# Optimization experiments

Measured on AMD Instinct MI355X. Metric: run time of the kernel, lower is better.

The kernel has to match this reference:

```python
import jax, jax.numpy as jnp
import numpy as np

B, M, D, HOPS = 32, 8192, 128, 3
NEG_BIG = -1e10  # matches (1 - memory_mask) * -1e10 in the original


def setup_inputs() -> dict:
    key = jax.random.key(0)
    k = jax.random.split(key, 6)
    return {
        "query_vector": jax.random.normal(k[0], (B, D), dtype=jnp.float32),
        # m_story[h] is the hop-h memory (already summed over token axis and gated upstream)
        "m_story": jax.random.normal(k[1], (HOPS + 1, B, M, D), dtype=jnp.float32),
        "global_pointer": jax.random.uniform(k[2], (B, M), dtype=jnp.float32),
        "local_attention": jax.random.uniform(k[3], (B, M), dtype=jnp.float32),
        "reason_mask": jax.random.randint(k[4], (B, M), 0, 2, dtype=jnp.int32),
        "memory_mask": jax.random.randint(k[5], (B, M), 0, 2, dtype=jnp.int32),
    }


def reference(query_vector, m_story, global_pointer, local_attention, reason_mask, memory_mask):
    # gating applied to both m_A and m_C every hop (ablationG off, attention=True)
    gate = (global_pointer * local_attention)[:, :, None]        # [B, M, 1]
    allowed = reason_mask.astype(bool)                           # rea=True: positions in `reason`
    mm = memory_mask.astype(jnp.float32)                         # [B, M]
    u = query_vector                                             # [B, D]
    n_hops = m_story.shape[0] - 1
    for hop in range(n_hops):
        m_A = m_story[hop] * gate                                # [B, M, D]
        prob_logits = jnp.einsum('bmd,bd->bm', m_A, u)           # [B, M]
        prob_logits = jnp.where(allowed, prob_logits, -jnp.inf)  # reason mask (vectorized double-loop)
        prob_logits = prob_logits + (1.0 - mm) * NEG_BIG
        prob_soft = jax.nn.softmax(prob_logits, axis=1)          # softmax over memory dim
        m_C = m_story[hop + 1] * gate                            # [B, M, D]
        o_k = jnp.einsum('bm,bmd->bd', prob_soft, m_C)           # [B, D]
        u = u + o_k
    return prob_soft, prob_logits, u
```

## Files before the change

### kernel.cpp

```cpp
#include <hip/hip_runtime.h>
#include <math.h>

constexpr int Bc = 32;
constexpr int Mc = 8192;
constexpr int Dc = 128;
constexpr int NHOPS = 3;
constexpr float NEGBIG = -1e10f;
constexpr float SENT = -3.0e38f;

constexpr int ROWS = 256;
constexpr int BLK_PER_B = Mc / ROWS;

__global__ __launch_bounds__(256) void k_init_u(const float* __restrict__ q,
                                                float* __restrict__ u) {
    int i = blockIdx.x * 256 + threadIdx.x;
    if (i < Bc * Dc) u[i] = q[i];
}

__global__ __launch_bounds__(256) void k_logits(
    const float* __restrict__ ms_hop,
    const float* __restrict__ u,
    const float* __restrict__ gp,
    const float* __restrict__ la,
    const int*   __restrict__ rmask,
    const int*   __restrict__ mmask,
    float* __restrict__ logits,
    float* __restrict__ ws_stats)
{
    const int b   = blockIdx.y;
    const int m0  = blockIdx.x * ROWS;
    const int tid = threadIdx.x;
    const int lane = tid & 31, grp = tid >> 5;
    const int wv = tid >> 6, wl = tid & 63;

    __shared__ alignas(16) float u_s[Dc];
    __shared__ float logit_s[ROWS];
    __shared__ float gate_s[ROWS];
    __shared__ float bias_s[ROWS];
    __shared__ short list_s[ROWS];
    __shared__ int   wcnt[4];
    __shared__ float red_s[256];

    if (tid < Dc) u_s[tid] = u[b * Dc + tid];
    const int idx = b * Mc + m0 + tid;
    const bool keep = rmask[idx] != 0;
    gate_s[tid]  = gp[idx] * la[idx];
    bias_s[tid]  = (1.0f - (float)mmask[idx]) * NEGBIG;
    logit_s[tid] = SENT;
    {
        unsigned long long bm_ = __ballot(keep);
        int pfx = __popcll(bm_ & ((1ull << wl) - 1ull));
        if (wl == 0) wcnt[wv] = __popcll(bm_);
        __syncthreads();
        int base = 0;
        for (int w2 = 0; w2 < wv; ++w2) base += wcnt[w2];
        if (keep) list_s[base + pfx] = (short)tid;
    }
    __syncthreads();
    const int cnt = wcnt[0] + wcnt[1] + wcnt[2] + wcnt[3];
    const float4 u4 = ((const float4*)u_s)[lane];

    int i = grp;
    for (; i + 8 < cnt; i += 16) {
        const int r0 = list_s[i], r1 = list_s[i + 8];
        const float4 v0 = ((const float4*)(ms_hop + (size_t)(m0 + r0) * Dc))[lane];
        const float4 v1 = ((const float4*)(ms_hop + (size_t)(m0 + r1) * Dc))[lane];
        float d0 = v0.x * u4.x + v0.y * u4.y + v0.z * u4.z + v0.w * u4.w;
        float d1 = v1.x * u4.x + v1.y * u4.y + v1.z * u4.z + v1.w * u4.w;
        #pragma unroll
        for (int off = 16; off > 0; off >>= 1) {
            d0 += __shfl_xor(d0, off, 32);
            d1 += __shfl_xor(d1, off, 32);
        }
        if (lane == 0) {
            logit_s[r0] = d0 * gate_s[r0] + bias_s[r0];
            logit_s[r1] = d1 * gate_s[r1] + bias_s[r1];
        }
    }
    for (; i < cnt; i += 8) {
        const int r0 = list_s[i];
        const float4 v0 = ((const float4*)(ms_hop + (size_t)(m0 + r0) * Dc))[lane];
        float d0 = v0.x * u4.x + v0.y * u4.y + v0.z * u4.z + v0.w * u4.w;
        #pragma unroll
        for (int off = 16; off > 0; off >>= 1) d0 += __shfl_xor(d0, off, 32);
        if (lane == 0) logit_s[r0] = d0 * gate_s[r0] + bias_s[r0];
    }
    __syncthreads();

    logits[idx] = logit_s[tid];
    red_s[tid] = logit_s[tid];
    __syncthreads();
    for (int s = 128; s > 0; s >>= 1) {
        if (tid < s) red_s[tid] = fmaxf(red_s[tid], red_s[tid + s]);
        __syncthreads();
    }
    const float M = red_s[0];
    __syncthreads();
    red_s[tid] = expf(logit_s[tid] - M);
    __syncthreads();
    for (int s = 128; s > 0; s >>= 1) {
        if (tid < s) red_s[tid] += red_s[tid + s];
        __syncthreads();
    }
    if (tid == 0) {
        const int blk = b * BLK_PER_B + blockIdx.x;
        ws_stats[blk * 2 + 0] = M;
        ws_stats[blk * 2 + 1] = red_s[0];
    }
}

__global__ __launch_bounds__(256) void k_accum(
    const float* __restrict__ ms_next,
    const float* __restrict__ logits,
    const float* __restrict__ gp,
    const float* __restrict__ la,
    const float* __restrict__ ws_stats,
    float* __restrict__ prob,
    float* __restrict__ u,
    int last)
{
    const int b   = blockIdx.y;
    const int m0  = blockIdx.x * ROWS;
    const int tid = threadIdx.x;
    const int lane = tid & 31, grp = tid >> 5;
    const int wv = tid >> 6, wl = tid & 63;

    __shared__ float w_s[ROWS];
    __shared__ short list_s[ROWS];
    __shared__ int   wcnt[4];
    __shared__ float sm_s[BLK_PER_B], ss_s[BLK_PER_B];
    __shared__ float bstat[2];
    __shared__ alignas(16) float acc_s[8 * Dc];

    if (tid < BLK_PER_B) {
        sm_s[tid] = ws_stats[(b * BLK_PER_B + tid) * 2 + 0];
        ss_s[tid] = ws_stats[(b * BLK_PER_B + tid) * 2 + 1];
    }
    __syncthreads();
    if (tid == 0) {
        float M = -INFINITY, S = 0.0f;
        for (int c = 0; c < BLK_PER_B; ++c) M = fmaxf(M, sm_s[c]);
        for (int c = 0; c < BLK_PER_B; ++c) S += ss_s[c] * expf(sm_s[c] - M);
        bstat[0] = M;
        bstat[1] = 1.0f / S;
    }
    __syncthreads();
    const float bm = bstat[0], inv = bstat[1];

    const int idx = b * Mc + m0 + tid;
    const float p = expf(logits[idx] - bm) * inv;
    if (last) prob[idx] = p;
    const float w = p * gp[idx] * la[idx];
    w_s[tid] = w;
    {
        const bool nz = (w != 0.0f);
        unsigned long long bm_ = __ballot(nz);
        int pfx = __popcll(bm_ & ((1ull << wl) - 1ull));
        if (wl == 0) wcnt[wv] = __popcll(bm_);
        __syncthreads();
        int base = 0;
        for (int w2 = 0; w2 < wv; ++w2) base += wcnt[w2];
        if (nz) list_s[base + pfx] = (short)tid;
    }
    __syncthreads();
    const int cnt = wcnt[0] + wcnt[1] + wcnt[2] + wcnt[3];

    float4 acc = make_float4(0.f, 0.f, 0.f, 0.f);
    int i = grp;
    for (; i + 8 < cnt; i += 16) {
        const int r0 = list_s[i], r1 = list_s[i + 8];
        const float w0 = w_s[r0], w1 = w_s[r1];
        const float4 v0 = ((const float4*)(ms_next + (size_t)(m0 + r0) * Dc))[lane];
        const float4 v1 = ((const float4*)(ms_next + (size_t)(m0 + r1) * Dc))[lane];
        acc.x += w0 * v0.x; acc.y += w0 * v0.y;
        acc.z += w0 * v0.z; acc.w += w0 * v0.w;
        acc.x += w1 * v1.x; acc.y += w1 * v1.y;
        acc.z += w1 * v1.z; acc.w += w1 * v1.w;
    }
    for (; i < cnt; i += 8) {
        const int r0 = list_s[i];
        const float w0 = w_s[r0];
        const float4 v0 = ((const float4*)(ms_next + (size_t)(m0 + r0) * Dc))[lane];
        acc.x += w0 * v0.x; acc.y += w0 * v0.y;
        acc.z += w0 * v0.z; acc.w += w0 * v0.w;
    }
    ((float4*)(acc_s + grp * Dc))[lane] = acc;
    __syncthreads();

    if (tid < Dc) {
        float s = 0.0f;
        #pragma unroll
        for (int g = 0; g < 8; ++g) s += acc_s[g * Dc + tid];
        atomicAdd(&u[b * Dc + tid], s);
    }
}

extern "C" void kernel_launch(void* const* d_in, const int* in_sizes, int n_in,
                              void* d_out, int out_size, void* d_ws,
                              size_t ws_size, hipStream_t stream) {
    const float* q  = (const float*)d_in[0];
    const float* ms = (const float*)d_in[1];
    const float* gp = (const float*)d_in[2];
    const float* la = (const float*)d_in[3];
    const int*   rm = (const int*)d_in[4];
    const int*   mm = (const int*)d_in[5];

    float* out_prob   = (float*)d_out;
    float* out_logits = out_prob + (size_t)Bc * Mc;
    float* out_u      = out_logits + (size_t)Bc * Mc;

    float* ws_stats = (float*)d_ws;

    k_init_u<<<dim3((Bc * Dc + 255) / 256), dim3(256), 0, stream>>>(q, out_u);

    for (int hop = 0; hop < NHOPS; ++hop) {
        const float* ms_h = ms + (size_t)hop       * Bc * Mc * Dc;
        const float* ms_n = ms + (size_t)(hop + 1) * Bc * Mc * Dc;
        const int last = (hop == NHOPS - 1) ? 1 : 0;

        k_logits<<<dim3(BLK_PER_B, Bc), dim3(256), 0, stream>>>(
            ms_h, out_u, gp, la, rm, mm, out_logits, ws_stats);
        k_accum<<<dim3(BLK_PER_B, Bc), dim3(256), 0, stream>>>(
            ms_n, out_logits, gp, la, ws_stats, out_prob, out_u, last);
    }
}
```

Measured before the change: 622.7 us.

## Fuse all hops into one cooperative persistent kernel with grid syncs

Replaces the init kernel and the six per-hop logits/accumulate launches with a single cooperative kernel. It keeps gate, bias, mask lists and logits in shared memory across hops and uses grid.sync between phases. It also swaps the tree reductions for wave shuffles and unrolls the row loops to four rows. This removes launch gaps and global round-trips of logits, gp and la, but needs all 1024 blocks co-resident and pays for several grid-wide barriers.

```diff
diff --git a/kernel.cpp b/kernel.cpp
--- a/kernel.cpp
+++ b/kernel.cpp
@@ -1,5 +1,8 @@
 #include <hip/hip_runtime.h>
+#include <hip/hip_cooperative_groups.h>
 #include <math.h>
+
+namespace cg = cooperative_groups;
 
 constexpr int Bc = 32;
 constexpr int Mc = 8192;
@@ -11,22 +14,19 @@
 constexpr int ROWS = 256;
 constexpr int BLK_PER_B = Mc / ROWS;
 
-__global__ __launch_bounds__(256) void k_init_u(const float* __restrict__ q,
-                                                float* __restrict__ u) {
-    int i = blockIdx.x * 256 + threadIdx.x;
-    if (i < Bc * Dc) u[i] = q[i];
-}
-
-__global__ __launch_bounds__(256) void k_logits(
-    const float* __restrict__ ms_hop,
-    const float* __restrict__ u,
+__global__ __launch_bounds__(256, 4) void k_fused(
+    const float* __restrict__ ms,
+    const float* __restrict__ q,
     const float* __restrict__ gp,
     const float* __restrict__ la,
     const int*   __restrict__ rmask,
     const int*   __restrict__ mmask,
-    float* __restrict__ logits,
+    float* __restrict__ out_prob,
+    float* __restrict__ out_logits,
+    float* __restrict__ u,
     float* __restrict__ ws_stats)
 {
+    cg::grid_group grid = cg::this_grid();
     const int b   = blockIdx.y;
     const int m0  = blockIdx.x * ROWS;
     const int tid = threadIdx.x;
@@ -34,19 +34,21 @@
     const int wv = tid >> 6, wl = tid & 63;
 
     __shared__ alignas(16) float u_s[Dc];
-    __shared__ float logit_s[ROWS];
     __shared__ float gate_s[ROWS];
     __shared__ float bias_s[ROWS];
+    __shared__ float logit_s[ROWS];
+    __shared__ float w_s[ROWS];
     __shared__ short list_s[ROWS];
-    __shared__ int   wcnt[4];
-    __shared__ float red_s[256];
-
-    if (tid < Dc) u_s[tid] = u[b * Dc + tid];
+    __shared__ short alist_s[ROWS];
+    __shared__ int   wcnt[4], awcnt[4];
+    __shared__ float red_s[8];
+    __shared__ float bstat[2];
+    __shared__ alignas(16) float acc_s[8 * Dc];
+
     const int idx = b * Mc + m0 + tid;
     const bool keep = rmask[idx] != 0;
-    gate_s[tid]  = gp[idx] * la[idx];
-    bias_s[tid]  = (1.0f - (float)mmask[idx]) * NEGBIG;
-    logit_s[tid] = SENT;
+    gate_s[tid] = gp[idx] * la[idx];
+    bias_s[tid] = (1.0f - (float)mmask[idx]) * NEGBIG;
     {
         unsigned long long bm_ = __ballot(keep);
         int pfx = __popcll(bm_ & ((1ull << wl) - 1ull));
@@ -56,142 +58,150 @@
         for (int w2 = 0; w2 < wv; ++w2) base += wcnt[w2];
         if (keep) list_s[base + pfx] = (short)tid;
     }
-    __syncthreads();
+    if (blockIdx.x == 0 && tid < Dc)
+        __hip_atomic_store(&u[b * Dc + tid], q[b * Dc + tid],
+                           __ATOMIC_RELAXED, __HIP_MEMORY_SCOPE_AGENT);
+    grid.sync();
     const int cnt = wcnt[0] + wcnt[1] + wcnt[2] + wcnt[3];
-    const float4 u4 = ((const float4*)u_s)[lane];
-
-    int i = grp;
-    for (; i + 8 < cnt; i += 16) {
-        const int r0 = list_s[i], r1 = list_s[i + 8];
-        const float4 v0 = ((const float4*)(ms_hop + (size_t)(m0 + r0) * Dc))[lane];
-        const float4 v1 = ((const float4*)(ms_hop + (size_t)(m0 + r1) * Dc))[lane];
-        float d0 = v0.x * u4.x + v0.y * u4.y + v0.z * u4.z + v0.w * u4.w;
-        float d1 = v1.x * u4.x + v1.y * u4.y + v1.z * u4.z + v1.w * u4.w;
+
+    for (int hop = 0; hop < NHOPS; ++hop) {
+        const float* ms_h = ms + (size_t)hop * Bc * Mc * Dc + (size_t)m0 * Dc;
+
+        if (tid < Dc)
+            u_s[tid] = __hip_atomic_load(&u[b * Dc + tid],
+                                         __ATOMIC_RELAXED, __HIP_MEMORY_SCOPE_AGENT);
+        logit_s[tid] = SENT;
+        __syncthreads();
+        const float4 u4 = ((const float4*)u_s)[lane];
+
+        int i = grp;
+        for (; i + 24 < cnt; i += 32) {
+            const int r0 = list_s[i],      r1 = list_s[i + 8];
+            const int r2 = list_s[i + 16], r3 = list_s[i + 24];
+            const float4 v0 = ((const float4*)(ms_h + (size_t)r0 * Dc))[lane];
+            const float4 v1 = ((const float4*)(ms_h + (size_t)r1 * Dc))[lane];
+            const float4 v2 = ((const float4*)(ms_h + (size_t)r2 * Dc))[lane];
+            const float4 v3 = ((const float4*)(ms_h + (size_t)r3 * Dc))[lane];
+            float d0 = v0.x * u4.x + v0.y * u4.y + v0.z * u4.z + v0.w * u4.w;
+            float d1 = v1.x * u4.x + v1.y * u4.y + v1.z * u4.z + v1.w * u4.w;
+            float d2 = v2.x * u4.x + v2.y * u4.y + v2.z * u4.z + v2.w * u4.w;
+            float d3 = v3.x * u4.x + v3.y * u4.y + v3.z * u4.z + v3.w * u4.w;
+            #pragma unroll
+            for (int off = 16; off > 0; off >>= 1) {
+                d0 += __shfl_xor(d0, off, 32);
+                d1 += __shfl_xor(d1, off, 32);
+                d2 += __shfl_xor(d2, off, 32);
+                d3 += __shfl_xor(d3, off, 32);
+            }
+            if (lane == 0) {
+                logit_s[r0] = d0 * gate_s[r0] + bias_s[r0];
+                logit_s[r1] = d1 * gate_s[r1] + bias_s[r1];
+                logit_s[r2] = d2 * gate_s[r2] + bias_s[r2];
+                logit_s[r3] = d3 * gate_s[r3] + bias_s[r3];
+            }
+        }
+        for (; i < cnt; i += 8) {
+            const int r0 = list_s[i];
+            const float4 v0 = ((const float4*)(ms_h + (size_t)r0 * Dc))[lane];
+            float d0 = v0.x * u4.x + v0.y * u4.y + v0.z * u4.z + v0.w * u4.w;
+            #pragma unroll
+            for (int off = 16; off > 0; off >>= 1) d0 += __shfl_xor(d0, off, 32);
+            if (lane == 0) logit_s[r0] = d0 * gate_s[r0] + bias_s[r0];
+        }
+        __syncthreads();
+
+        const float v = logit_s[tid];
+        float mx = v;
         #pragma unroll
-        for (int off = 16; off > 0; off >>= 1) {
-            d0 += __shfl_xor(d0, off, 32);
-            d1 += __shfl_xor(d1, off, 32);
-        }
-        if (lane == 0) {
-            logit_s[r0] = d0 * gate_s[r0] + bias_s[r0];
-            logit_s[r1] = d1 * gate_s[r1] + bias_s[r1];
-        }
-    }
-    for (; i < cnt; i += 8) {
-        const int r0 = list_s[i];
-        const float4 v0 = ((const float4*)(ms_hop + (size_t)(m0 + r0) * Dc))[lane];
-        float d0 = v0.x * u4.x + v0.y * u4.y + v0.z * u4.z + v0.w * u4.w;
+        for (int off = 32; off > 0; off >>= 1) mx = fmaxf(mx, __shfl_xor(mx, off));
+        if (wl == 0) red_s[wv] = mx;
+        __syncthreads();
+        const float M = fmaxf(fmaxf(red_s[0], red_s[1]), fmaxf(red_s[2], red_s[3]));
+        float e = expf(v - M);
         #pragma unroll
-        for (int off = 16; off > 0; off >>= 1) d0 += __shfl_xor(d0, off, 32);
-        if (lane == 0) logit_s[r0] = d0 * gate_s[r0] + bias_s[r0];
-    }
-    __syncthreads();
-
-    logits[idx] = logit_s[tid];
-    red_s[tid] = logit_s[tid];
-    __syncthreads();
-    for (int s = 128; s > 0; s >>= 1) {
-        if (tid < s) red_s[tid] = fmaxf(red_s[tid], red_s[tid + s]);
-        __syncthreads();
-    }
-    const float M = red_s[0];
-    __syncthreads();
-    red_s[tid] = expf(logit_s[tid] - M);
-    __syncthreads();
-    for (int s = 128; s > 0; s >>= 1) {
-        if (tid < s) red_s[tid] += red_s[tid + s];
-        __syncthreads();
-    }
-    if (tid == 0) {
-        const int blk = b * BLK_PER_B + blockIdx.x;
-        ws_stats[blk * 2 + 0] = M;
-        ws_stats[blk * 2 + 1] = red_s[0];
-    }
-}
-
-__global__ __launch_bounds__(256) void k_accum(
-    const float* __restrict__ ms_next,
-    const float* __restrict__ logits,
-    const float* __restrict__ gp,
-    const float* __restrict__ la,
-    const float* __restrict__ ws_stats,
-    float* __restrict__ prob,
-    float* __restrict__ u,
-    int last)
-{
-    const int b   = blockIdx.y;
-    const int m0  = blockIdx.x * ROWS;
-    const int tid = threadIdx.x;
-    const int lane = tid & 31, grp = tid >> 5;
-    const int wv = tid >> 6, wl = tid & 63;
-
-    __shared__ float w_s[ROWS];
-    __shared__ short list_s[ROWS];
-    __shared__ int   wcnt[4];
-    __shared__ float sm_s[BLK_PER_B], ss_s[BLK_PER_B];
-    __shared__ float bstat[2];
-    __shared__ alignas(16) float acc_s[8 * Dc];
-
-    if (tid < BLK_PER_B) {
-        sm_s[tid] = ws_stats[(b * BLK_PER_B + tid) * 2 + 0];
-        ss_s[tid] = ws_stats[(b * BLK_PER_B + tid) * 2 + 1];
-    }
-    __syncthreads();
-    if (tid == 0) {
-        float M = -INFINITY, S = 0.0f;
-        for (int c = 0; c < BLK_PER_B; ++c) M = fmaxf(M, sm_s[c]);
-        for (int c = 0; c < BLK_PER_B; ++c) S += ss_s[c] * expf(sm_s[c] - M);
-        bstat[0] = M;
-        bstat[1] = 1.0f / S;
-    }
-    __syncthreads();
-    const float bm = bstat[0], inv = bstat[1];
-
-    const int idx = b * Mc + m0 + tid;
-    const float p = expf(logits[idx] - bm) * inv;
-    if (last) prob[idx] = p;
-    const float w = p * gp[idx] * la[idx];
-    w_s[tid] = w;
-    {
-        const bool nz = (w != 0.0f);
-        unsigned long long bm_ = __ballot(nz);
-        int pfx = __popcll(bm_ & ((1ull << wl) - 1ull));
-        if (wl == 0) wcnt[wv] = __popcll(bm_);
-        __syncthreads();
-        int base = 0;
-        for (int w2 = 0; w2 < wv; ++w2) base += wcnt[w2];
-        if (nz) list_s[base + pfx] = (short)tid;
-    }
-    __syncthreads();
-    const int cnt = wcnt[0] + wcnt[1] + wcnt[2] + wcnt[3];
-
-    float4 acc = make_float4(0.f, 0.f, 0.f, 0.f);
-    int i = grp;
-    for (; i + 8 < cnt; i += 16) {
-        const int r0 = list_s[i], r1 = list_s[i + 8];
-        const float w0 = w_s[r0], w1 = w_s[r1];
-        const float4 v0 = ((const float4*)(ms_next + (size_t)(m0 + r0) * Dc))[lane];
-        const float4 v1 = ((const float4*)(ms_next + (size_t)(m0 + r1) * Dc))[lane];
-        acc.x += w0 * v0.x; acc.y += w0 * v0.y;
-        acc.z += w0 * v0.z; acc.w += w0 * v0.w;
-        acc.x += w1 * v1.x; acc.y += w1 * v1.y;
-        acc.z += w1 * v1.z; acc.w += w1 * v1.w;
-    }
-    for (; i < cnt; i += 8) {
-        const int r0 = list_s[i];
-        const float w0 = w_s[r0];
-        const float4 v0 = ((const float4*)(ms_next + (size_t)(m0 + r0) * Dc))[lane];
-        acc.x += w0 * v0.x; acc.y += w0 * v0.y;
-        acc.z += w0 * v0.z; acc.w += w0 * v0.w;
-    }
-    ((float4*)(acc_s + grp * Dc))[lane] = acc;
-    __syncthreads();
-
-    if (tid < Dc) {
-        float s = 0.0f;
-        #pragma unroll
-        for (int g = 0; g < 8; ++g) s += acc_s[g * Dc + tid];
-        atomicAdd(&u[b * Dc + tid], s);
+        for (int off = 32; off > 0; off >>= 1) e += __shfl_xor(e, off);
+        if (wl == 0) red_s[4 + wv] = e;
+        if (hop == NHOPS - 1) out_logits[idx] = v;
+        __syncthreads();
+        if (tid == 0) {
+            const int blk = b * BLK_PER_B + blockIdx.x;
+            __hip_atomic_store(&ws_stats[blk * 2 + 0], M,
+                               __ATOMIC_RELAXED, __HIP_MEMORY_SCOPE_AGENT);
+            __hip_atomic_store(&ws_stats[blk * 2 + 1],
+                               red_s[4] + red_s[5] + red_s[6] + red_s[7],
+                               __ATOMIC_RELAXED, __HIP_MEMORY_SCOPE_AGENT);
+        }
+        grid.sync();
+
+        if (wv == 0) {
+            float sm = (wl < BLK_PER_B)
+                ? __hip_atomic_load(&ws_stats[(b * BLK_PER_B + wl) * 2 + 0],
+                                    __ATOMIC_RELAXED, __HIP_MEMORY_SCOPE_AGENT)
+                : -INFINITY;
+            float ss = (wl < BLK_PER_B)
+                ? __hip_atomic_load(&ws_stats[(b * BLK_PER_B + wl) * 2 + 1],
+                                    __ATOMIC_RELAXED, __HIP_MEMORY_SCOPE_AGENT)
+                : 0.0f;
+            float Mg = sm;
+            #pragma unroll
+            for (int off = 32; off > 0; off >>= 1) Mg = fmaxf(Mg, __shfl_xor(Mg, off));
+            float t = ss * expf(sm - Mg);
+            #pragma unroll
+            for (int off = 32; off > 0; off >>= 1) t += __shfl_xor(t, off);
+            if (wl == 0) { bstat[0] = Mg; bstat[1] = 1.0f / t; }
+        }
+        __syncthreads();
+        const float bm = bstat[0], inv = bstat[1];
+
+        const float p = expf(logit_s[tid] - bm) * inv;
+        if (hop == NHOPS - 1) out_prob[idx] = p;
+        const float w = p * gate_s[tid];
+        w_s[tid] = w;
+        {
+            const bool nz = (w != 0.0f);
+            unsigned long long bm_ = __ballot(nz);
+            int pfx = __popcll(bm_ & ((1ull << wl) - 1ull));
+            if (wl == 0) awcnt[wv] = __popcll(bm_);
+            __syncthreads();
+            int base2 = 0;
+            for (int w2 = 0; w2 < wv; ++w2) base2 += awcnt[w2];
+            if (nz) alist_s[base2 + pfx] = (short)tid;
+        }
+        __syncthreads();
+        const int acnt = awcnt[0] + awcnt[1] + awcnt[2] + awcnt[3];
+
+        const float* ms_n = ms + (size_t)(hop + 1) * Bc * Mc * Dc + (size_t)m0 * Dc;
+        float4 acc = make_float4(0.f, 0.f, 0.f, 0.f);
+        int j = grp;
+        for (; j + 24 < acnt; j += 32) {
+            const int r0 = alist_s[j],      r1 = alist_s[j + 8];
+            const int r2 = alist_s[j + 16], r3 = alist_s[j + 24];
+            const float w0 = w_s[r0], w1 = w_s[r1], w2 = w_s[r2], w3 = w_s[r3];
+            const float4 v0 = ((const float4*)(ms_n + (size_t)r0 * Dc))[lane];
+            const float4 v1 = ((const float4*)(ms_n + (size_t)r1 * Dc))[lane];
+            const float4 v2 = ((const float4*)(ms_n + (size_t)r2 * Dc))[lane];
+            const float4 v3 = ((const float4*)(ms_n + (size_t)r3 * Dc))[lane];
+            acc.x += w0 * v0.x; acc.y += w0 * v0.y; acc.z += w0 * v0.z; acc.w += w0 * v0.w;
+            acc.x += w1 * v1.x; acc.y += w1 * v1.y; acc.z += w1 * v1.z; acc.w += w1 * v1.w;
+            acc.x += w2 * v2.x; acc.y += w2 * v2.y; acc.z += w2 * v2.z; acc.w += w2 * v2.w;
+            acc.x += w3 * v3.x; acc.y += w3 * v3.y; acc.z += w3 * v3.z; acc.w += w3 * v3.w;
+        }
+        for (; j < acnt; j += 8) {
+            const int r0 = alist_s[j];
+            const float w0 = w_s[r0];
+            const float4 v0 = ((const float4*)(ms_n + (size_t)r0 * Dc))[lane];
+            acc.x += w0 * v0.x; acc.y += w0 * v0.y; acc.z += w0 * v0.z; acc.w += w0 * v0.w;
+        }
+        ((float4*)(acc_s + grp * Dc))[lane] = acc;
+        __syncthreads();
+
+        if (tid < Dc) {
+            float sacc = 0.0f;
+            #pragma unroll
+            for (int g = 0; g < 8; ++g) sacc += acc_s[g * Dc + tid];
+            atomicAdd(&u[b * Dc + tid], sacc);
+        }
+        if (hop < NHOPS - 1) grid.sync();
     }
 }
 
@@ -211,16 +221,13 @@
 
     float* ws_stats = (float*)d_ws;
 
-    k_init_u<<<dim3((Bc * Dc + 255) / 256), dim3(256), 0, stream>>>(q, out_u);
-
-    for (int hop = 0; hop < NHOPS; ++hop) {
-        const float* ms_h = ms + (size_t)hop       * Bc * Mc * Dc;
-        const float* ms_n = ms + (size_t)(hop + 1) * Bc * Mc * Dc;
-        const int last = (hop == NHOPS - 1) ? 1 : 0;
-
-        k_logits<<<dim3(BLK_PER_B, Bc), dim3(256), 0, stream>>>(
-            ms_h, out_u, gp, la, rm, mm, out_logits, ws_stats);
-        k_accum<<<dim3(BLK_PER_B, Bc), dim3(256), 0, stream>>>(
-            ms_n, out_logits, gp, la, ws_stats, out_prob, out_u, last);
-    }
+    void* args[] = {
+        (void*)&ms, (void*)&q, (void*)&gp, (void*)&la,
+        (void*)&rm, (void*)&mm,
+        (void*)&out_prob, (void*)&out_logits, (void*)&out_u,
+        (void*)&ws_stats
+    };
+    hipLaunchCooperativeKernel((void*)k_fused,
+                               dim3(BLK_PER_B, Bc), dim3(256),
+                               args, 0, stream);
 }
```

After: 1.269 ms. +103.9%, slower.
